# Optimization experiments

Measured on AMD Instinct MI355X. Metric: run time of the kernel, lower is better.

Reference implementation:

```python
import jax, jax.numpy as jnp
import numpy as np

B, S, D_MODEL, H = 2, 2048, 1024, 16
D = D_MODEL // H  # per-head dim


def setup_inputs() -> dict:
    key = jax.random.key(0)
    ks = jax.random.split(key, 12)
    s = 1.0 / np.sqrt(D_MODEL)
    return {
        "pre_q": jax.random.normal(ks[0], (B, S, D_MODEL), jnp.float32),
        "pre_k": jax.random.normal(ks[1], (B, S, D_MODEL), jnp.float32),
        "pre_v": jax.random.normal(ks[2], (B, S, D_MODEL), jnp.float32),
        "mask": jnp.ones((1, S, S), dtype=bool),
        # per-head QKV projections, stacked: [H, d_model, d] (x @ W + b form)
        "Wq": jax.random.normal(ks[3], (H, D_MODEL, D), jnp.float32) * s,
        "bq": jax.random.normal(ks[4], (H, D), jnp.float32) * s,
        "Wk": jax.random.normal(ks[5], (H, D_MODEL, D), jnp.float32) * s,
        "bk": jax.random.normal(ks[6], (H, D), jnp.float32) * s,
        "Wv": jax.random.normal(ks[7], (H, D_MODEL, D), jnp.float32) * s,
        "bv": jax.random.normal(ks[8], (H, D), jnp.float32) * s,
        "Wo": jax.random.normal(ks[9], (D_MODEL, D_MODEL), jnp.float32) * s,
        "bo": jax.random.normal(ks[10], (D_MODEL,), jnp.float32) * s,
    }


def reference(pre_q, pre_k, pre_v, mask, Wq, bq, Wk, bk, Wv, bv, Wo, bo):
    # Batched per-head projections: [B,S,Dm] x [H,Dm,d] -> [B,H,S,d]
    Q = jnp.einsum("bsm,hmd->bhsd", pre_q, Wq) + bq[None, :, None, :]
    K = jnp.einsum("bsm,hmd->bhsd", pre_k, Wk) + bk[None, :, None, :]
    V = jnp.einsum("bsm,hmd->bhsd", pre_v, Wv) + bv[None, :, None, :]

    scores = jnp.einsum("bhqd,bhkd->bhqk", Q, K) / jnp.sqrt(jnp.asarray(D, Q.dtype))
    # mask broadcasts [1,S,S] -> [B,H,S,S]; masked positions get -1e9
    scores = jnp.where(mask[:, None, :, :], scores, jnp.asarray(-1e9, scores.dtype))
    attn = jax.nn.softmax(scores, axis=-1)  # [B,H,Sq,Sk]
    out_heads = jnp.einsum("bhqk,bhkd->bhqd", attn, V)

    # concat heads: [B,S,H*d] (head order matches torch cat over head list)
    concat = out_heads.transpose(0, 2, 1, 3).reshape(B, S, D_MODEL)
    out = concat @ Wo + bo  # dropout is identity in eval mode

    # torch: stack([H,B,Sq,Sk]).permute(0,3,1,2) -> [H, Sk, B, Sq]
    attn_weights = attn.transpose(1, 0, 2, 3).transpose(0, 3, 1, 2)
    return out, attn_weights
```

## Files before the change

### kernel.cpp

```cpp
#include <hip/hip_runtime.h>

typedef __bf16 bhalf8 __attribute__((ext_vector_type(8)));
typedef float f32x4 __attribute__((ext_vector_type(4)));
typedef short short4v __attribute__((ext_vector_type(4)));
typedef short short8v __attribute__((ext_vector_type(8)));

#define DEVI static __device__ __forceinline__

DEVI short f2bf(float f) {
  union { float f; unsigned u; } x;
  x.f = f;
  unsigned r = x.u + 0x7FFF + ((x.u >> 16) & 1);
  return (short)(r >> 16);
}
DEVI bhalf8 ld8s(const short* p) { return *(const bhalf8*)p; }

constexpr float QSCALE = 0.18033688011112042f;

__global__ void transpose_k(const float* __restrict__ in, short* __restrict__ out,
                            int R, int C) {
  __shared__ short t[64][65];
  const int r0 = blockIdx.x * 64, c0 = blockIdx.y * 64;
  const size_t boff = (size_t)blockIdx.z * R * C;
  const int tid = threadIdx.x;
  for (int p = 0; p < 16; ++p) {
    int e = p * 256 + tid;
    int r = e >> 6, c = e & 63;
    t[r][c] = f2bf(in[boff + (size_t)(r0 + r) * C + (c0 + c)]);
  }
  __syncthreads();
  for (int p = 0; p < 16; ++p) {
    int e = p * 256 + tid;
    int c = e >> 6, r = e & 63;
    out[boff + (size_t)(c0 + c) * R + (r0 + r)] = t[r][c];
  }
}

template <int MODE, bool ABF16>
__launch_bounds__(256, 2) __global__
void gemm_bias_k(const void* __restrict__ Av, const short* __restrict__ Bt,
                 const float* __restrict__ bias, void* __restrict__ dstv) {
  constexpr int LDA = 72;
  constexpr int LDE = 136;
  __shared__ __align__(16) char smem[36864];
  short* As = (short*)smem;
  short* Bs = (short*)(smem + 18432);
  short* Es = (short*)smem;
  const float* Af = (const float*)Av;
  const short* Ah = (const short*)Av;

  const int r0 = blockIdx.x * 128, n0 = blockIdx.y * 128;
  const int tid = threadIdx.x;
  const int w = tid >> 6, l = tid & 63;
  const int wr = (w >> 1) * 64, wn = (w & 1) * 64;
  const int lq = l & 15, quad = l >> 4;
  const int sc = tid & 7, srow = tid >> 3;

  f32x4 acc[4][4] = {};
  f32x4 a0[4], a1[4];
  bhalf8 ar[4], br[4];

  auto LOADT = [&](int m0) {
    for (int i = 0; i < 4; ++i) {
      int row = srow + i * 32;
      if constexpr (ABF16) {
        ar[i] = ld8s(Ah + (size_t)(r0 + row) * 1024 + m0 + sc * 8);
      } else {
        const float* ap = Af + (size_t)(r0 + row) * 1024 + m0 + sc * 8;
        a0[i] = *(const f32x4*)ap;
        a1[i] = *(const f32x4*)(ap + 4);
      }
      br[i] = ld8s(Bt + (size_t)(n0 + row) * 1024 + m0 + sc * 8);
    }
  };

  LOADT(0);
  for (int kt = 0; kt < 16; ++kt) {
    __syncthreads();
    for (int i = 0; i < 4; ++i) {
      int row = srow + i * 32;
      if constexpr (ABF16) {
        *(bhalf8*)&As[row * LDA + sc * 8] = ar[i];
      } else {
        short8v v;
        for (int e = 0; e < 4; ++e) v[e] = f2bf(a0[i][e]);
        for (int e = 0; e < 4; ++e) v[4 + e] = f2bf(a1[i][e]);
        *(short8v*)&As[row * LDA + sc * 8] = v;
      }
      *(bhalf8*)&Bs[row * LDA + sc * 8] = br[i];
    }
    __syncthreads();
    if (kt < 15) LOADT((kt + 1) * 64);
    __builtin_amdgcn_s_setprio(1);
    for (int kk = 0; kk < 2; ++kk) {
      bhalf8 af[4], bfr[4];
      for (int i = 0; i < 4; ++i)
        af[i] = *(const bhalf8*)&As[(wr + i * 16 + lq) * LDA + kk * 32 + quad * 8];
      for (int j = 0; j < 4; ++j)
        bfr[j] = *(const bhalf8*)&Bs[(wn + j * 16 + lq) * LDA + kk * 32 + quad * 8];
      for (int i = 0; i < 4; ++i)
        for (int j = 0; j < 4; ++j)
          acc[i][j] = __builtin_amdgcn_mfma_f32_16x16x32_bf16(af[i], bfr[j], acc[i][j], 0, 0, 0);
    }
    __builtin_amdgcn_s_setprio(0);
  }

  if (MODE == 3) {
    float* dst = (float*)dstv;
    for (int i = 0; i < 4; ++i)
      for (int j = 0; j < 4; ++j) {
        int n = wn + j * 16 + lq;
        float bv = bias[n0 + n];
        for (int rg = 0; rg < 4; ++rg) {
          int r = wr + i * 16 + quad * 4 + rg;
          dst[(size_t)(r0 + r) * 1024 + n0 + n] = acc[i][j][rg] + bv;
        }
      }
    return;
  }

  short* dst = (short*)dstv;
  __syncthreads();
  if (MODE != 2) {
    for (int i = 0; i < 4; ++i)
      for (int j = 0; j < 4; ++j) {
        int n = wn + j * 16 + lq;
        float bv = bias[n0 + n];
        for (int rg = 0; rg < 4; ++rg) {
          int r = wr + i * 16 + quad * 4 + rg;
          float y = acc[i][j][rg] + bv;
          if (MODE == 0) y *= QSCALE;
          Es[r * LDE + n] = f2bf(y);
        }
      }
  } else {
    for (int i = 0; i < 4; ++i)
      for (int j = 0; j < 4; ++j) {
        int n = wn + j * 16 + lq;
        float bv = bias[n0 + n];
        short4v pk;
        for (int rg = 0; rg < 4; ++rg) pk[rg] = f2bf(acc[i][j][rg] + bv);
        *(short4v*)&Es[n * LDE + wr + i * 16 + quad * 4] = pk;
      }
  }
  __syncthreads();
  const int c = tid & 15, rr = tid >> 4;
  for (int p = 0; p < 8; ++p) {
    int r = rr + p * 16;
    bhalf8 v = *(const bhalf8*)&Es[r * LDE + c * 8];
    if (MODE == 0 || MODE == 1) {
      int b = r0 >> 11, s = (r0 & 2047) + r;
      int n = n0 + c * 8, hh = n >> 6, d = n & 63;
      *(bhalf8*)(dst + (((size_t)(b * 16 + hh) * 2048 + s) << 6) + d) = v;
    } else {
      int n = n0 + r, hh = n >> 6, d = n & 63;
      int b = r0 >> 11, s = (r0 & 2047) + c * 8;
      *(bhalf8*)(dst + (((size_t)(b * 16 + hh) * 64 + d) << 11) + s) = v;
    }
  }
}

__launch_bounds__(256, 2) __global__
void attn_k(const short* __restrict__ Qh, const short* __restrict__ Kh,
            const short* __restrict__ Vt, float* __restrict__ attn_out,
            short* __restrict__ concat) {
  constexpr int LDK = 72, LDV = 136, LDPW = 72, LDO = 68;
  __shared__ __align__(16) char smem[74240];
  short* Ks = (short*)smem;
  short* Vs = (short*)(smem + 18432);
  short* Pw = (short*)(smem + 35840);
  float* Of = (float*)smem;
  float* lsum = (float*)(smem + 72704);
  float* rl = (float*)(smem + 73728);

  const int q0 = blockIdx.x * 128;
  const int bh = blockIdx.y;
  const int b = bh >> 4, h = bh & 15;
  const short* Qp = Qh + ((size_t)bh << 11) * 64;
  const short* Kp = Kh + ((size_t)bh << 11) * 64;
  const short* Vp = Vt + ((size_t)bh << 6) * 2048;

  const int tid = threadIdx.x;
  const int w = tid >> 6, l = tid & 63;
  const int lq = l & 15, quad = l >> 4;
  const int wk = w >> 1, wq = w & 1;
  const int sc = tid & 7, srow = tid >> 3;

  bhalf8 qf[4][2];
  for (int qt = 0; qt < 4; ++qt)
    for (int kk = 0; kk < 2; ++kk)
      qf[qt][kk] = ld8s(Qp + (size_t)(q0 + wq * 64 + qt * 16 + lq) * 64 + kk * 32 + quad * 8);

  short* Pm = Pw + w * (64 * LDPW);

  float rs[4] = {0.f, 0.f, 0.f, 0.f};
  f32x4 oacc[4][4] = {};
  for (int kt = 0; kt < 16; ++kt) {
    const int k0 = kt * 128;
    __syncthreads();
    for (int i = 0; i < 4; ++i) {
      int row = srow + i * 32;
      *(bhalf8*)&Ks[row * LDK + sc * 8] = ld8s(Kp + (size_t)(k0 + row) * 64 + sc * 8);
    }
    {
      int c2 = tid & 15, d2 = tid >> 4;
      for (int i = 0; i < 4; ++i) {
        int d = d2 + i * 16;
        *(bhalf8*)&Vs[d * LDV + c2 * 8] = ld8s(Vp + ((size_t)d << 11) + k0 + c2 * 8);
      }
    }
    __syncthreads();
    f32x4 sacc[4][4] = {};
    __builtin_amdgcn_s_setprio(1);
    for (int kk = 0; kk < 2; ++kk) {
      bhalf8 kf[4];
      for (int mt = 0; mt < 4; ++mt)
        kf[mt] = *(const bhalf8*)&Ks[(wk * 64 + mt * 16 + lq) * LDK + kk * 32 + quad * 8];
      for (int mt = 0; mt < 4; ++mt)
        for (int qt = 0; qt < 4; ++qt)
          sacc[mt][qt] = __builtin_amdgcn_mfma_f32_16x16x32_bf16(kf[mt], qf[qt][kk], sacc[mt][qt], 0, 0, 0);
    }
    __builtin_amdgcn_s_setprio(0);
    for (int mt = 0; mt < 4; ++mt)
      for (int qt = 0; qt < 4; ++qt) {
        short4v pk;
        for (int rg = 0; rg < 4; ++rg) {
          float p = exp2f(sacc[mt][qt][rg]);
          rs[qt] += p;
          pk[rg] = f2bf(p);
        }
        *(short4v*)&Pm[(qt * 16 + lq) * LDPW + mt * 16 + quad * 4] = pk;
      }
    __builtin_amdgcn_s_setprio(1);
    for (int kki = 0; kki < 2; ++kki) {
      bhalf8 pf[4], vf[4];
      for (int qt = 0; qt < 4; ++qt)
        pf[qt] = *(const bhalf8*)&Pm[(qt * 16 + lq) * LDPW + kki * 32 + quad * 8];
      for (int dt = 0; dt < 4; ++dt)
        vf[dt] = *(const bhalf8*)&Vs[(dt * 16 + lq) * LDV + wk * 64 + kki * 32 + quad * 8];
      for (int qt = 0; qt < 4; ++qt)
        for (int dt = 0; dt < 4; ++dt)
          oacc[qt][dt] = __builtin_amdgcn_mfma_f32_16x16x32_bf16(pf[qt], vf[dt], oacc[qt][dt], 0, 0, 0);
    }
    __builtin_amdgcn_s_setprio(0);
  }

  for (int qt = 0; qt < 4; ++qt) {
    float v = rs[qt];
    v += __shfl_xor(v, 16);
    v += __shfl_xor(v, 32);
    rs[qt] = v;
  }
  if (quad == 0)
    for (int qt = 0; qt < 4; ++qt)
      lsum[wk * 128 + wq * 64 + qt * 16 + lq] = rs[qt];
  __syncthreads();
  if (tid < 128) rl[tid] = 1.0f / (lsum[tid] + lsum[128 + tid]);
  __syncthreads();
  float rlv[4];
  for (int qt = 0; qt < 4; ++qt) rlv[qt] = rl[wq * 64 + qt * 16 + lq];

  if (wk == 1)
    for (int qt = 0; qt < 4; ++qt)
      for (int dt = 0; dt < 4; ++dt)
        for (int rg = 0; rg < 4; ++rg)
          Of[(wq * 64 + qt * 16 + quad * 4 + rg) * LDO + dt * 16 + lq] = oacc[qt][dt][rg];
  __syncthreads();
  if (wk == 0)
    for (int qt = 0; qt < 4; ++qt)
      for (int dt = 0; dt < 4; ++dt)
        for (int rg = 0; rg < 4; ++rg) {
          int idx = (wq * 64 + qt * 16 + quad * 4 + rg) * LDO + dt * 16 + lq;
          Of[idx] += oacc[qt][dt][rg];
        }
  __syncthreads();
  {
    int cg = tid & 7, rb = tid >> 3;
    for (int p = 0; p < 4; ++p) {
      int r = rb + p * 32;
      float sc2 = rl[r];
      const float* src = &Of[r * LDO + cg * 8];
      short8v v8;
      for (int e = 0; e < 8; ++e) v8[e] = f2bf(src[e] * sc2);
      *(short8v*)&concat[((size_t)(b * 2048 + q0 + r) << 10) + h * 64 + cg * 8] = v8;
    }
  }

  bhalf8 kreg[4];
  for (int i = 0; i < 4; ++i)
    kreg[i] = ld8s(Kp + (size_t)(srow + i * 32) * 64 + sc * 8);
  for (int kt = 0; kt < 16; ++kt) {
    const int k0 = kt * 128;
    __syncthreads();
    for (int i = 0; i < 4; ++i)
      *(bhalf8*)&Ks[(srow + i * 32) * LDK + sc * 8] = kreg[i];
    __syncthreads();
    if (kt < 15)
      for (int i = 0; i < 4; ++i)
        kreg[i] = ld8s(Kp + (size_t)(k0 + 128 + srow + i * 32) * 64 + sc * 8);
    f32x4 sacc[4][4] = {};
    __builtin_amdgcn_s_setprio(1);
    for (int kk = 0; kk < 2; ++kk) {
      bhalf8 kf[4];
      for (int mt = 0; mt < 4; ++mt)
        kf[mt] = *(const bhalf8*)&Ks[(wk * 64 + mt * 16 + lq) * LDK + kk * 32 + quad * 8];
      for (int mt = 0; mt < 4; ++mt)
        for (int qt = 0; qt < 4; ++qt)
          sacc[mt][qt] = __builtin_amdgcn_mfma_f32_16x16x32_bf16(kf[mt], qf[qt][kk], sacc[mt][qt], 0, 0, 0);
    }
    __builtin_amdgcn_s_setprio(0);
    for (int mt = 0; mt < 4; ++mt) {
      int krow = wk * 64 + mt * 16 + quad * 4;
      for (int qt = 0; qt < 4; ++qt) {
        int q = wq * 64 + qt * 16 + lq;
        size_t gbase = ((size_t)(h * 2048 + k0 + krow) * 2 + b) * 2048 + q0 + q;
        for (int rg = 0; rg < 4; ++rg)
          attn_out[gbase + (size_t)rg * 4096] = exp2f(sacc[mt][qt][rg]) * rlv[qt];
      }
    }
  }
}

extern "C" void kernel_launch(void* const* d_in, const int* in_sizes, int n_in,
                              void* d_out, int out_size, void* d_ws, size_t ws_size,
                              hipStream_t stream) {
  (void)in_sizes; (void)n_in; (void)out_size; (void)ws_size;
  const float* pre_q = (const float*)d_in[0];
  const float* pre_k = (const float*)d_in[1];
  const float* pre_v = (const float*)d_in[2];
  const float* Wq = (const float*)d_in[4];
  const float* bq = (const float*)d_in[5];
  const float* Wk = (const float*)d_in[6];
  const float* bk = (const float*)d_in[7];
  const float* Wv = (const float*)d_in[8];
  const float* bv = (const float*)d_in[9];
  const float* Wo = (const float*)d_in[10];
  const float* bo = (const float*)d_in[11];

  float* out  = (float*)d_out;
  float* attn = out + 4194304;

  char* W = (char*)d_ws;
  short* wtq = (short*)(W);
  short* wtk = (short*)(W + (2u << 20));
  short* wtv = (short*)(W + (4u << 20));
  short* wot = (short*)(W + (6u << 20));
  short* qh  = (short*)(W + (8u << 20));
  short* kh  = (short*)(W + (16u << 20));
  short* vt  = (short*)(W + (24u << 20));
  short* cc  = (short*)(W + (32u << 20));

  transpose_k<<<dim3(16, 1, 16), 256, 0, stream>>>(Wq, wtq, 1024, 64);
  transpose_k<<<dim3(16, 1, 16), 256, 0, stream>>>(Wk, wtk, 1024, 64);
  transpose_k<<<dim3(16, 1, 16), 256, 0, stream>>>(Wv, wtv, 1024, 64);
  transpose_k<<<dim3(16, 16, 1), 256, 0, stream>>>(Wo, wot, 1024, 1024);
  gemm_bias_k<0, false><<<dim3(32, 8), 256, 0, stream>>>(pre_q, wtq, bq, qh);
  gemm_bias_k<1, false><<<dim3(32, 8), 256, 0, stream>>>(pre_k, wtk, bk, kh);
  gemm_bias_k<2, false><<<dim3(32, 8), 256, 0, stream>>>(pre_v, wtv, bv, vt);
  attn_k<<<dim3(16, 32), 256, 0, stream>>>(qh, kh, vt, attn, cc);
  gemm_bias_k<3, true><<<dim3(32, 8), 256, 0, stream>>>(cc, wot, bo, out);
}
```

Before: 759.8 us.

## Batch QKV launches, swizzle attention grid, vectorize nontemporal attn-weight stores

Merges the three weight transposes into one launch and the three QKV projection GEMMs into one 3D-grid launch, which cuts launch overhead and improves GPU fill. The attention kernel now uses a 1D swizzled block index and double-buffers K in shared memory, reusing the P region, so one barrier per tile is dropped. It also swaps the QK MFMA operand order so each lane holds 4 consecutive query columns. That lets the large attn_weights output be written as 16-byte nontemporal vector stores instead of scalar strided stores. Reusing the Pw region as the second K buffer depends on it being free at that point.

```diff
diff --git a/kernel.cpp b/kernel.cpp
--- a/kernel.cpp
+++ b/kernel.cpp
@@ -36,18 +36,36 @@
   }
 }
 
-template <int MODE, bool ABF16>
+__global__ void transpose3_k(const float* __restrict__ i0, const float* __restrict__ i1,
+                             const float* __restrict__ i2, short* __restrict__ o0,
+                             short* __restrict__ o1, short* __restrict__ o2) {
+  __shared__ short t[64][65];
+  const int sel = blockIdx.z >> 4, zb = blockIdx.z & 15;
+  const float* in = sel == 0 ? i0 : sel == 1 ? i1 : i2;
+  short* out = sel == 0 ? o0 : sel == 1 ? o1 : o2;
+  const int r0 = blockIdx.x * 64;
+  const size_t boff = (size_t)zb * 1024 * 64;
+  const int tid = threadIdx.x;
+  for (int p = 0; p < 16; ++p) {
+    int e = p * 256 + tid;
+    int r = e >> 6, c = e & 63;
+    t[r][c] = f2bf(in[boff + (size_t)(r0 + r) * 64 + c]);
+  }
+  __syncthreads();
+  for (int p = 0; p < 16; ++p) {
+    int e = p * 256 + tid;
+    int c = e >> 6, r = e & 63;
+    out[boff + (size_t)c * 1024 + (r0 + r)] = t[r][c];
+  }
+}
+
 __launch_bounds__(256, 2) __global__
-void gemm_bias_k(const void* __restrict__ Av, const short* __restrict__ Bt,
-                 const float* __restrict__ bias, void* __restrict__ dstv) {
+void out_gemm_k(const short* __restrict__ Ah, const short* __restrict__ Bt,
+                const float* __restrict__ bias, float* __restrict__ dst) {
   constexpr int LDA = 72;
-  constexpr int LDE = 136;
   __shared__ __align__(16) char smem[36864];
   short* As = (short*)smem;
   short* Bs = (short*)(smem + 18432);
-  short* Es = (short*)smem;
-  const float* Af = (const float*)Av;
-  const short* Ah = (const short*)Av;
 
   const int r0 = blockIdx.x * 128, n0 = blockIdx.y * 128;
   const int tid = threadIdx.x;
@@ -57,19 +75,11 @@
   const int sc = tid & 7, srow = tid >> 3;
 
   f32x4 acc[4][4] = {};
-  f32x4 a0[4], a1[4];
   bhalf8 ar[4], br[4];
-
   auto LOADT = [&](int m0) {
     for (int i = 0; i < 4; ++i) {
       int row = srow + i * 32;
-      if constexpr (ABF16) {
-        ar[i] = ld8s(Ah + (size_t)(r0 + row) * 1024 + m0 + sc * 8);
-      } else {
-        const float* ap = Af + (size_t)(r0 + row) * 1024 + m0 + sc * 8;
-        a0[i] = *(const f32x4*)ap;
-        a1[i] = *(const f32x4*)(ap + 4);
-      }
+      ar[i] = ld8s(Ah + (size_t)(r0 + row) * 1024 + m0 + sc * 8);
       br[i] = ld8s(Bt + (size_t)(n0 + row) * 1024 + m0 + sc * 8);
     }
   };
@@ -79,14 +89,7 @@
     __syncthreads();
     for (int i = 0; i < 4; ++i) {
       int row = srow + i * 32;
-      if constexpr (ABF16) {
-        *(bhalf8*)&As[row * LDA + sc * 8] = ar[i];
-      } else {
-        short8v v;
-        for (int e = 0; e < 4; ++e) v[e] = f2bf(a0[i][e]);
-        for (int e = 0; e < 4; ++e) v[4 + e] = f2bf(a1[i][e]);
-        *(short8v*)&As[row * LDA + sc * 8] = v;
-      }
+      *(bhalf8*)&As[row * LDA + sc * 8] = ar[i];
       *(bhalf8*)&Bs[row * LDA + sc * 8] = br[i];
     }
     __syncthreads();
@@ -104,24 +107,86 @@
     }
     __builtin_amdgcn_s_setprio(0);
   }
-
-  if (MODE == 3) {
-    float* dst = (float*)dstv;
-    for (int i = 0; i < 4; ++i)
-      for (int j = 0; j < 4; ++j) {
-        int n = wn + j * 16 + lq;
-        float bv = bias[n0 + n];
-        for (int rg = 0; rg < 4; ++rg) {
-          int r = wr + i * 16 + quad * 4 + rg;
-          dst[(size_t)(r0 + r) * 1024 + n0 + n] = acc[i][j][rg] + bv;
-        }
-      }
-    return;
-  }
-
-  short* dst = (short*)dstv;
-  __syncthreads();
-  if (MODE != 2) {
+  for (int i = 0; i < 4; ++i)
+    for (int j = 0; j < 4; ++j) {
+      int n = wn + j * 16 + lq;
+      float bv = bias[n0 + n];
+      for (int rg = 0; rg < 4; ++rg) {
+        int r = wr + i * 16 + quad * 4 + rg;
+        dst[(size_t)(r0 + r) * 1024 + n0 + n] = acc[i][j][rg] + bv;
+      }
+    }
+}
+
+__launch_bounds__(256, 2) __global__
+void qkv_k(const float* __restrict__ Aq, const float* __restrict__ Ak,
+           const float* __restrict__ Avv, const short* __restrict__ Bq,
+           const short* __restrict__ Bk, const short* __restrict__ Bv,
+           const float* __restrict__ biq, const float* __restrict__ bik,
+           const float* __restrict__ biv, short* __restrict__ dq,
+           short* __restrict__ dk, short* __restrict__ dv) {
+  constexpr int LDA = 72;
+  constexpr int LDE = 136;
+  __shared__ __align__(16) char smem[36864];
+  short* As = (short*)smem;
+  short* Bs = (short*)(smem + 18432);
+  short* Es = (short*)smem;
+
+  const int mode = blockIdx.z;
+  const float* A = mode == 0 ? Aq : mode == 1 ? Ak : Avv;
+  const short* Bt = mode == 0 ? Bq : mode == 1 ? Bk : Bv;
+  const float* bias = mode == 0 ? biq : mode == 1 ? bik : biv;
+  short* dst = mode == 0 ? dq : mode == 1 ? dk : dv;
+
+  const int r0 = blockIdx.x * 128, n0 = blockIdx.y * 128;
+  const int tid = threadIdx.x;
+  const int w = tid >> 6, l = tid & 63;
+  const int wr = (w >> 1) * 64, wn = (w & 1) * 64;
+  const int lq = l & 15, quad = l >> 4;
+  const int sc = tid & 7, srow = tid >> 3;
+
+  f32x4 acc[4][4] = {};
+  f32x4 a0[4], a1[4];
+  bhalf8 br[4];
+  auto LOADT = [&](int m0) {
+    for (int i = 0; i < 4; ++i) {
+      int row = srow + i * 32;
+      const float* ap = A + (size_t)(r0 + row) * 1024 + m0 + sc * 8;
+      a0[i] = *(const f32x4*)ap;
+      a1[i] = *(const f32x4*)(ap + 4);
+      br[i] = ld8s(Bt + (size_t)(n0 + row) * 1024 + m0 + sc * 8);
+    }
+  };
+
+  LOADT(0);
+  for (int kt = 0; kt < 16; ++kt) {
+    __syncthreads();
+    for (int i = 0; i < 4; ++i) {
+      int row = srow + i * 32;
+      short8v v;
+      for (int e = 0; e < 4; ++e) v[e] = f2bf(a0[i][e]);
+      for (int e = 0; e < 4; ++e) v[4 + e] = f2bf(a1[i][e]);
+      *(short8v*)&As[row * LDA + sc * 8] = v;
+      *(bhalf8*)&Bs[row * LDA + sc * 8] = br[i];
+    }
+    __syncthreads();
+    if (kt < 15) LOADT((kt + 1) * 64);
+    __builtin_amdgcn_s_setprio(1);
+    for (int kk = 0; kk < 2; ++kk) {
+      bhalf8 af[4], bfr[4];
+      for (int i = 0; i < 4; ++i)
+        af[i] = *(const bhalf8*)&As[(wr + i * 16 + lq) * LDA + kk * 32 + quad * 8];
+      for (int j = 0; j < 4; ++j)
+        bfr[j] = *(const bhalf8*)&Bs[(wn + j * 16 + lq) * LDA + kk * 32 + quad * 8];
+      for (int i = 0; i < 4; ++i)
+        for (int j = 0; j < 4; ++j)
+          acc[i][j] = __builtin_amdgcn_mfma_f32_16x16x32_bf16(af[i], bfr[j], acc[i][j], 0, 0, 0);
+    }
+    __builtin_amdgcn_s_setprio(0);
+  }
+
+  __syncthreads();
+  if (mode != 2) {
     for (int i = 0; i < 4; ++i)
       for (int j = 0; j < 4; ++j) {
         int n = wn + j * 16 + lq;
@@ -129,7 +194,7 @@
         for (int rg = 0; rg < 4; ++rg) {
           int r = wr + i * 16 + quad * 4 + rg;
           float y = acc[i][j][rg] + bv;
-          if (MODE == 0) y *= QSCALE;
+          if (mode == 0) y *= QSCALE;
           Es[r * LDE + n] = f2bf(y);
         }
       }
@@ -148,7 +213,7 @@
   for (int p = 0; p < 8; ++p) {
     int r = rr + p * 16;
     bhalf8 v = *(const bhalf8*)&Es[r * LDE + c * 8];
-    if (MODE == 0 || MODE == 1) {
+    if (mode != 2) {
       int b = r0 >> 11, s = (r0 & 2047) + r;
       int n = n0 + c * 8, hh = n >> 6, d = n & 63;
       *(bhalf8*)(dst + (((size_t)(b * 16 + hh) * 2048 + s) << 6) + d) = v;
@@ -173,8 +238,10 @@
   float* lsum = (float*)(smem + 72704);
   float* rl = (float*)(smem + 73728);
 
-  const int q0 = blockIdx.x * 128;
-  const int bh = blockIdx.y;
+  const int bid = blockIdx.x;
+  const int swz = (bid & 7) * 64 + (bid >> 3);
+  const int q0 = (swz & 15) * 128;
+  const int bh = swz >> 4;
   const int b = bh >> 4, h = bh & 15;
   const short* Qp = Qh + ((size_t)bh << 11) * 64;
   const short* Kp = Kh + ((size_t)bh << 11) * 64;
@@ -257,8 +324,6 @@
   __syncthreads();
   if (tid < 128) rl[tid] = 1.0f / (lsum[tid] + lsum[128 + tid]);
   __syncthreads();
-  float rlv[4];
-  for (int qt = 0; qt < 4; ++qt) rlv[qt] = rl[wq * 64 + qt * 16 + lq];
 
   if (wk == 1)
     for (int qt = 0; qt < 4; ++qt)
@@ -286,14 +351,20 @@
     }
   }
 
+  f32x4 rlq[4];
+  for (int qt = 0; qt < 4; ++qt)
+    rlq[qt] = *(const f32x4*)&rl[wq * 64 + qt * 16 + quad * 4];
   bhalf8 kreg[4];
   for (int i = 0; i < 4; ++i)
     kreg[i] = ld8s(Kp + (size_t)(srow + i * 32) * 64 + sc * 8);
+  short* ksb0 = Ks;
+  short* ksb1 = Pw;
+  __syncthreads();
   for (int kt = 0; kt < 16; ++kt) {
     const int k0 = kt * 128;
-    __syncthreads();
+    short* kb = (kt & 1) ? ksb1 : ksb0;
     for (int i = 0; i < 4; ++i)
-      *(bhalf8*)&Ks[(srow + i * 32) * LDK + sc * 8] = kreg[i];
+      *(bhalf8*)&kb[(srow + i * 32) * LDK + sc * 8] = kreg[i];
     __syncthreads();
     if (kt < 15)
       for (int i = 0; i < 4; ++i)
@@ -303,19 +374,21 @@
     for (int kk = 0; kk < 2; ++kk) {
       bhalf8 kf[4];
       for (int mt = 0; mt < 4; ++mt)
-        kf[mt] = *(const bhalf8*)&Ks[(wk * 64 + mt * 16 + lq) * LDK + kk * 32 + quad * 8];
-      for (int mt = 0; mt < 4; ++mt)
-        for (int qt = 0; qt < 4; ++qt)
-          sacc[mt][qt] = __builtin_amdgcn_mfma_f32_16x16x32_bf16(kf[mt], qf[qt][kk], sacc[mt][qt], 0, 0, 0);
+        kf[mt] = *(const bhalf8*)&kb[(wk * 64 + mt * 16 + lq) * LDK + kk * 32 + quad * 8];
+      for (int qt = 0; qt < 4; ++qt)
+        for (int mt = 0; mt < 4; ++mt)
+          sacc[qt][mt] = __builtin_amdgcn_mfma_f32_16x16x32_bf16(qf[qt][kk], kf[mt], sacc[qt][mt], 0, 0, 0);
     }
     __builtin_amdgcn_s_setprio(0);
     for (int mt = 0; mt < 4; ++mt) {
-      int krow = wk * 64 + mt * 16 + quad * 4;
+      int k = wk * 64 + mt * 16 + lq;
       for (int qt = 0; qt < 4; ++qt) {
-        int q = wq * 64 + qt * 16 + lq;
-        size_t gbase = ((size_t)(h * 2048 + k0 + krow) * 2 + b) * 2048 + q0 + q;
+        int qb = wq * 64 + qt * 16 + quad * 4;
+        f32x4 pv;
         for (int rg = 0; rg < 4; ++rg)
-          attn_out[gbase + (size_t)rg * 4096] = exp2f(sacc[mt][qt][rg]) * rlv[qt];
+          pv[rg] = exp2f(sacc[qt][mt][rg]) * rlq[qt][rg];
+        float* dp = attn_out + ((size_t)(h * 2048 + k0 + k) * 2 + b) * 2048 + q0 + qb;
+        __builtin_nontemporal_store(pv, (f32x4*)dp);
       }
     }
   }
@@ -350,13 +423,10 @@
   short* vt  = (short*)(W + (24u << 20));
   short* cc  = (short*)(W + (32u << 20));
 
-  transpose_k<<<dim3(16, 1, 16), 256, 0, stream>>>(Wq, wtq, 1024, 64);
-  transpose_k<<<dim3(16, 1, 16), 256, 0, stream>>>(Wk, wtk, 1024, 64);
-  transpose_k<<<dim3(16, 1, 16), 256, 0, stream>>>(Wv, wtv, 1024, 64);
+  transpose3_k<<<dim3(16, 1, 48), 256, 0, stream>>>(Wq, Wk, Wv, wtq, wtk, wtv);
   transpose_k<<<dim3(16, 16, 1), 256, 0, stream>>>(Wo, wot, 1024, 1024);
-  gemm_bias_k<0, false><<<dim3(32, 8), 256, 0, stream>>>(pre_q, wtq, bq, qh);
-  gemm_bias_k<1, false><<<dim3(32, 8), 256, 0, stream>>>(pre_k, wtk, bk, kh);
-  gemm_bias_k<2, false><<<dim3(32, 8), 256, 0, stream>>>(pre_v, wtv, bv, vt);
-  attn_k<<<dim3(16, 32), 256, 0, stream>>>(qh, kh, vt, attn, cc);
-  gemm_bias_k<3, true><<<dim3(32, 8), 256, 0, stream>>>(cc, wot, bo, out);
-}
+  qkv_k<<<dim3(32, 8, 3), 256, 0, stream>>>(pre_q, pre_k, pre_v, wtq, wtk, wtv,
+                                            bq, bk, bv, qh, kh, vt);
+  attn_k<<<dim3(512), 256, 0, stream>>>(qh, kh, vt, attn, cc);
+  out_gemm_k<<<dim3(32, 8), 256, 0, stream>>>(cc, wot, bo, out);
+}
```

After: 775.0 us. No clear change (+2.0%).
